# Kernel tuning notes

Hardware: AMD Instinct MI355X
Metric: run time of the kernel (lower is better)

The kernel has to match this reference:

```python
import jax, jax.numpy as jnp
import numpy as np

N = 4096
INP_DIM = 256
EMB_DIM = 256
ALPHA = 0.01  # LeakyReLU negative slope
NEG_INF = -9.0e15


def _xavier(key, shape, gain=1.414):
    fan_in, fan_out = shape[0], shape[1]
    limit = gain * np.sqrt(6.0 / (fan_in + fan_out))
    return jax.random.uniform(key, shape, jnp.float32, -limit, limit)


def setup_inputs() -> dict:
    key = jax.random.key(0)
    ks = jax.random.split(key, 9)
    inp = {
        "input": jax.random.normal(ks[0], (N, INP_DIM), jnp.float32),
        "adj": jax.random.randint(ks[1], (N, N), 0, 2, jnp.int32),
        "W0": _xavier(ks[2], (INP_DIM, EMB_DIM)),
        "W1": _xavier(ks[3], (EMB_DIM, EMB_DIM)),
        "a1": _xavier(ks[4], (2 * EMB_DIM, 1)),
        "W2": _xavier(ks[5], (EMB_DIM, EMB_DIM)),
        "a2": _xavier(ks[6], (2 * EMB_DIM, 1)),
        "W3": _xavier(ks[7], (EMB_DIM, EMB_DIM)),
        "a3": _xavier(ks[8], (2 * EMB_DIM, 1)),
    }
    return inp


def _gat_layer(h, adj, W, a):
    # h: [N, F_in], W: [F_in, F], a: [2F, 1]
    Wh = h @ W                       # [N, F]
    F_out = Wh.shape[1]
    # e_ij = leakyrelu([Wh_i || Wh_j] @ a) = leakyrelu(Wh_i@a1 + Wh_j@a2)
    f1 = Wh @ a[:F_out]              # [N, 1]
    f2 = Wh @ a[F_out:]              # [N, 1]
    e = jax.nn.leaky_relu(f1 + f2.T, ALPHA)            # [N, N]
    att = jnp.where(adj > 0, e, NEG_INF)
    att = jax.nn.softmax(att, axis=1)                    # masked softmax over neighbors
    h_prime = att @ Wh                                   # [N, F]
    return jax.nn.elu(h_prime)                           # concat=True -> ELU


def reference(input, adj, W0, W1, a1, W2, a2, W3, a3):
    h = input @ W0                   # GAT-level projection
    h = _gat_layer(h, adj, W1, a1)
    h = _gat_layer(h, adj, W2, a2)
    h = _gat_layer(h, adj, W3, a3)
    return h
```

## Files before the change

### kernel.cpp

```cpp
#include <hip/hip_runtime.h>
#include <hip/hip_bf16.h>
#include <hip/hip_fp16.h>
#include <cstdint>
#include <cstddef>

#define NN 4096
#define FD 256
#define WPR 64

typedef __attribute__((ext_vector_type(8))) unsigned short ushort8v;
typedef __attribute__((ext_vector_type(4))) unsigned short ushort4v;
typedef __attribute__((ext_vector_type(8))) short short8;
typedef __attribute__((ext_vector_type(4))) float float4v;

#define C1 30.0f
#define C2 0.3f

static __device__ __forceinline__ unsigned short f2bf(float x) {
    union { float f; unsigned int u; } v; v.f = x;
    unsigned int r = v.u + 0x7FFFu + ((v.u >> 16) & 1u);
    return (unsigned short)(r >> 16);
}

static __device__ __forceinline__ short8 as_s8(ushort8v v) {
    union { ushort8v u; short8 s; } x; x.u = v; return x.s;
}

static __device__ __forceinline__ void gl_lds16(const unsigned short* g, unsigned short* l) {
    __builtin_amdgcn_global_load_lds(
        (const __attribute__((address_space(1))) unsigned int*)g,
        (__attribute__((address_space(3))) unsigned int*)l,
        16, 0, 0);
}

__global__ __launch_bounds__(256) void setup(const int* __restrict__ adj,
                                             const float* __restrict__ input,
                                             const float* __restrict__ W0, const float* __restrict__ W1,
                                             const float* __restrict__ W2, const float* __restrict__ W3,
                                             unsigned long long* __restrict__ bits,
                                             unsigned short* __restrict__ hb,
                                             unsigned short* __restrict__ Wbt,
                                             float* __restrict__ f1f2) {
    const int b = blockIdx.x;
    const int t = threadIdx.x;
    if (b < 4096) {
        const int wave = t >> 6, lane = t & 63;
        const int* arow = adj + (size_t)b * NN;
        #pragma unroll
        for (int it = 0; it < NN / 256; ++it) {
            int j = it * 256 + wave * 64 + lane;
            unsigned long long m = __ballot(arow[j] > 0);
            if (lane == 0) bits[(size_t)b * WPR + (it * 4 + wave)] = m;
        }
        hb[(size_t)b * 256 + t] = f2bf(input[(size_t)b * 256 + t]);
    } else if (b < 5120) {
        int idx = (b - 4096) * 256 + t;
        int mat = idx >> 16;
        int within = idx & 65535;
        int n = within >> 8, k = within & 255;
        const float* W = (mat == 0) ? W0 : (mat == 1) ? W1 : (mat == 2) ? W2 : W3;
        Wbt[idx] = f2bf(W[k * 256 + n]);
    } else {
        #pragma unroll
        for (int i = 0; i < 24; ++i) {
            int pos = i * 1024 + (b - 5120) * 256 + t;
            f1f2[pos] = 0.f;
        }
    }
}

__global__ __launch_bounds__(256) void proj_gemm(const unsigned short* __restrict__ A,
                                                 const unsigned short* __restrict__ Bt,
                                                 const float* __restrict__ av,
                                                 float* __restrict__ f1f2,
                                                 unsigned short* __restrict__ Cbt,
                                                 unsigned short* __restrict__ Crow) {
    const int t = threadIdx.x;
    const int bm = blockIdx.x >> 2, bn = blockIdx.x & 3;
    const int m0 = bm * 32, n0 = bn * 64;
    __shared__ unsigned short As[32 * 264];
    __shared__ unsigned short Bs[64 * 264];
    const int lane = t & 63, wave = t >> 6;
    const int wm = (wave >> 1) * 16, wn = (wave & 1) * 32;
    const int g = lane >> 4, ml = lane & 15;
    {
        int ar = t >> 3, ac0 = (t & 7) * 8;
        #pragma unroll
        for (int i = 0; i < 4; ++i) {
            int col = ac0 + i * 64;
            *(ushort8v*)&As[ar * 264 + col] = *(const ushort8v*)&A[(size_t)(m0 + ar) * 256 + col];
        }
        int br = t >> 2, bc0 = (t & 3) * 8;
        #pragma unroll
        for (int i = 0; i < 8; ++i) {
            int col = bc0 + i * 32;
            *(ushort8v*)&Bs[br * 264 + col] = *(const ushort8v*)&Bt[(size_t)(n0 + br) * 256 + col];
        }
    }
    __syncthreads();
    float4v acc[2] = {{0.f,0.f,0.f,0.f},{0.f,0.f,0.f,0.f}};
    #pragma unroll
    for (int kk = 0; kk < 256; kk += 32) {
        const int kc = kk + g * 8;
        short8 a = as_s8(*(const ushort8v*)&As[(wm + ml) * 264 + kc]);
        #pragma unroll
        for (int fn = 0; fn < 2; ++fn) {
            short8 b = as_s8(*(const ushort8v*)&Bs[(wn + fn * 16 + ml) * 264 + kc]);
            acc[fn] = __builtin_amdgcn_mfma_f32_16x16x32_bf16(a, b, acc[fn], 0, 0, 0);
        }
    }

    const int rb = wm + g * 4;
    if (Crow) {
        #pragma unroll
        for (int fn = 0; fn < 2; ++fn)
            #pragma unroll
            for (int r = 0; r < 4; ++r)
                Crow[(size_t)(m0 + rb + r) * 256 + n0 + wn + fn * 16 + ml] = f2bf(acc[fn][r]);
    }

    if (f1f2) {
        float a1c[2], a2c[2];
        #pragma unroll
        for (int fn = 0; fn < 2; ++fn) {
            a1c[fn] = av[n0 + wn + fn * 16 + ml];
            a2c[fn] = av[256 + n0 + wn + fn * 16 + ml];
        }
        #pragma unroll
        for (int r = 0; r < 4; ++r) {
            float s1 = acc[0][r] * a1c[0] + acc[1][r] * a1c[1];
            float s2 = acc[0][r] * a2c[0] + acc[1][r] * a2c[1];
            #pragma unroll
            for (int off = 1; off < 16; off <<= 1) {
                s1 += __shfl_xor(s1, off, 64);
                s2 += __shfl_xor(s2, off, 64);
            }
            if (ml == 0) {
                int row = m0 + rb + r;
                atomicAdd(&f1f2[row], s1);
                atomicAdd(&f1f2[4096 + row], s2);
            }
        }
    }

    if (Cbt) {
        unsigned short* T = As;
        __syncthreads();
        #pragma unroll
        for (int fn = 0; fn < 2; ++fn)
            #pragma unroll
            for (int r = 0; r < 4; ++r)
                T[(wn + fn * 16 + ml) * 40 + rb + r] = f2bf(acc[fn][r]);
        __syncthreads();
        const int tr = t >> 2, tc = (t & 3) * 8;
        *(ushort8v*)&Cbt[(size_t)(n0 + tr) * 4096 + m0 + tc] = *(const ushort8v*)&T[tr * 40 + tc];
    }
}

__global__ __launch_bounds__(256) void rowcoef(const unsigned long long* __restrict__ bits,
                                               const float* __restrict__ f1f2,
                                               float4* __restrict__ rowco,
                                               float2* __restrict__ tab2g) {
    __shared__ float2 tl[4096];
    const int t = threadIdx.x;
    const float* f2p = f1f2 + 4096;
    #pragma unroll
    for (int i = 0; i < 16; ++i) {
        float v = f2p[i * 256 + t];
        float2 pr = make_float2(__expf(v - C1), __expf(0.01f * v - C2));
        tl[i * 256 + t] = pr;
        if (blockIdx.x == 0) tab2g[i * 256 + t] = pr;
    }
    __syncthreads();
    const int lane = t & 63, wave = t >> 6;
    for (int rr = 0; rr < 2; ++rr) {
        const int row = blockIdx.x * 8 + wave * 2 + rr;
        const unsigned long long wl = bits[(size_t)row * WPR + lane];
        const float f1r = f1f2[row];
        const float th = __expf(-f1r - C1);
        float mx = 0.f, S1 = 0.f, S2 = 0.f;
        #pragma unroll 16
        for (int b = 0; b < 64; ++b) {
            unsigned long long w = __shfl(wl, b, 64);
            bool bit = (w >> lane) & 1ULL;
            float2 v = tl[b * 64 + lane];
            float ebm = bit ? v.x : 0.f;
            mx = fmaxf(mx, ebm);
            bool cond = v.x > th;
            S1 += (bit && cond)  ? v.x : 0.f;
            S2 += (bit && !cond) ? v.y : 0.f;
        }
        #pragma unroll
        for (int off = 1; off < 64; off <<= 1) {
            mx = fmaxf(mx, __shfl_xor(mx, off, 64));
            S1 += __shfl_xor(S1, off, 64);
            S2 += __shfl_xor(S2, off, 64);
        }
        if (lane == 0) {
            float M  = C1 + __logf(mx);
            float fm_ = f1r + M;
            float m  = fm_ > 0.f ? fm_ : 0.01f * fm_;
            float alpha = __expf(fminf(f1r + C1 - m, 60.f));
            float gamma = __expf(fminf(0.01f * (f1r + C1) - m, 60.f));
            float inv = 1.0f / (alpha * S1 + gamma * S2);
            rowco[row] = make_float4(alpha * inv, gamma * inv, th, 0.f);
        }
    }
}

template<int NSTEPS>
__global__ __launch_bounds__(256, 3) void att_gemm(const unsigned long long* __restrict__ bits,
                                                   const float4* __restrict__ rowco,
                                                   const float* __restrict__ tab2f,
                                                   const unsigned short* __restrict__ Bt,
                                                   unsigned short* __restrict__ parth) {
    const int t = threadIdx.x;
    const int bm = blockIdx.x & 31;
    const int bn = (blockIdx.x >> 5) & 1;
    const int ks = blockIdx.x >> 6;
    const int m0 = bm * 128, n0 = bn * 128;
    const int k0 = ks * (NSTEPS * 32);
    __shared__ unsigned short Bs[2][128 * 32];
    const int lane = t & 63, wave = t >> 6;
    const int g = lane >> 4, ml = lane & 15;

    const int drow = lane >> 2, dcol = ((lane & 3) ^ (lane >> 4)) * 8;
    const unsigned short* dsrc0 = Bt + (size_t)(n0 + wave * 16 + drow) * 4096 + dcol;
    const unsigned short* dsrc1 = dsrc0 + (size_t)64 * 4096;
    unsigned short* dst0 = &Bs[0][wave * 512];
    unsigned short* dst1 = &Bs[0][2048 + wave * 512];
    unsigned short* dst0b = &Bs[1][wave * 512];
    unsigned short* dst1b = &Bs[1][2048 + wave * 512];

    float pA[2], pG[2];
    unsigned long long wpre[2][NSTEPS / 2];
    #pragma unroll
    for (int fm = 0; fm < 2; ++fm) {
        int row = m0 + wave * 32 + fm * 16 + ml;
        float4 rc = rowco[row];
        pA[fm] = rc.x; pG[fm] = rc.y;
        const unsigned long long* brow = bits + (size_t)row * WPR + (k0 >> 6);
        #pragma unroll
        for (int w = 0; w < NSTEPS / 2; ++w) wpre[fm][w] = brow[w];
    }

    float4v acc[2][8];
    #pragma unroll
    for (int i = 0; i < 2; ++i)
        #pragma unroll
        for (int j = 0; j < 8; ++j) acc[i][j] = (float4v){0.f, 0.f, 0.f, 0.f};

    float4v tq0, tq1, tq2, tq3;
    {
        gl_lds16(dsrc0 + k0, dst0);
        gl_lds16(dsrc1 + k0, dst1);
        const float4v* q = (const float4v*)&tab2f[2 * (k0 + g * 8)];
        tq0 = q[0]; tq1 = q[1]; tq2 = q[2]; tq3 = q[3];
    }
    __syncthreads();

    const int rdoff = ((g ^ (ml >> 2)) & 3) * 8;

    #pragma unroll
    for (int i = 0; i < NSTEPS; ++i) {
        const int kk = k0 + i * 32;
        const int p = i & 1;
        float4v nt0, nt1, nt2, nt3;
        if (i + 1 < NSTEPS) {
            gl_lds16(dsrc0 + kk + 32, p ? dst0 : dst0b);
            gl_lds16(dsrc1 + kk + 32, p ? dst1 : dst1b);
            const float4v* q = (const float4v*)&tab2f[2 * (kk + 32 + g * 8)];
            nt0 = q[0]; nt1 = q[1]; nt2 = q[2]; nt3 = q[3];
        }
        const int sh = (i & 1) * 32 + g * 8;
        short8 afr[2];
        #pragma unroll
        for (int fm = 0; fm < 2; ++fm) {
            unsigned int wh = (unsigned int)(wpre[fm][i >> 1] >> sh);
            ushort8v af;
            #pragma unroll
            for (int jj = 0; jj < 4; ++jj) {
                float4v v = (jj == 0) ? tq0 : (jj == 1) ? tq1 : (jj == 2) ? tq2 : tq3;
                float x0 = fmaxf(pA[fm] * v[0], pG[fm] * v[1]);
                float x1 = fmaxf(pA[fm] * v[2], pG[fm] * v[3]);
                x0 = ((wh >> (2 * jj)) & 1u)     ? x0 : 0.f;
                x1 = ((wh >> (2 * jj + 1)) & 1u) ? x1 : 0.f;
                union { __hip_bfloat162 b2; unsigned int u; } cv;
                cv.b2 = __float22bfloat162_rn(make_float2(x0, x1));
                ((unsigned int*)&af)[jj] = cv.u;
            }
            afr[fm] = as_s8(af);
        }
        #pragma unroll
        for (int fn = 0; fn < 8; ++fn) {
            short8 b = as_s8(*(const ushort8v*)&Bs[p][(fn * 16 + ml) * 32 + rdoff]);
            acc[0][fn] = __builtin_amdgcn_mfma_f32_16x16x32_bf16(afr[0], b, acc[0][fn], 0, 0, 0);
            acc[1][fn] = __builtin_amdgcn_mfma_f32_16x16x32_bf16(afr[1], b, acc[1][fn], 0, 0, 0);
        }
        if (i + 1 < NSTEPS) {
            __syncthreads();
            tq0 = nt0; tq1 = nt1; tq2 = nt2; tq3 = nt3;
        }
    }

    unsigned short* pbase = parth + ((size_t)ks << 20) + (size_t)(bm * 2 + bn) * 16384;
    #pragma unroll
    for (int fm = 0; fm < 2; ++fm)
        #pragma unroll
        for (int fn = 0; fn < 8; ++fn) {
            ushort4v v4;
            #pragma unroll
            for (int r = 0; r < 4; ++r) {
                __half h = __float2half(acc[fm][fn][r]);
                v4[r] = *(unsigned short*)&h;
            }
            *(ushort4v*)&pbase[((wave * 16 + fm * 8 + fn) * 64 + lane) * 4] = v4;
        }
}

template<int NS>
__global__ __launch_bounds__(256) void fused_rp(const unsigned short* __restrict__ parth,
                                                const unsigned short* __restrict__ Bt,
                                                const float* __restrict__ av,
                                                float* __restrict__ f1f2,
                                                unsigned short* __restrict__ Cbt) {
    const int t = threadIdx.x;
    const int m0 = blockIdx.x * 16;
    __shared__ unsigned short hA[16 * 280];
    __shared__ unsigned short T[256 * 24];

    const int bmP = m0 >> 7;
    const int wavea = (m0 >> 5) & 3;
    const int fmP = (m0 >> 4) & 1;
    const int bn = t >> 7, fnc = (t >> 4) & 7;
    const int widx = wavea * 16 + fmP * 8 + fnc;
    const size_t cbase = (size_t)(bmP * 2 + bn) * 16384 + (size_t)widx * 256 + (t & 15) * 16;
    float s[16];
    #pragma unroll
    for (int e = 0; e < 16; ++e) s[e] = 0.f;
    #pragma unroll
    for (int sp = 0; sp < NS; ++sp) {
        const unsigned short* p = &parth[((size_t)sp << 20) + cbase];
        ushort8v v0 = *(const ushort8v*)p;
        ushort8v v1 = *(const ushort8v*)(p + 8);
        #pragma unroll
        for (int e = 0; e < 8; ++e) {
            unsigned short u0 = v0[e], u1 = v1[e];
            s[e]     += __half2float(*(__half*)&u0);
            s[8 + e] += __half2float(*(__half*)&u1);
        }
    }
    const int gq = (t & 15) >> 2;
    const int colb = bn * 128 + fnc * 16 + (t & 3) * 4;
    #pragma unroll
    for (int r = 0; r < 4; ++r) {
        ushort4v w4;
        #pragma unroll
        for (int c = 0; c < 4; ++c) {
            float x = s[c * 4 + r];
            x = x > 0.f ? x : (__expf(x) - 1.f);
            w4[c] = f2bf(x);
        }
        *(ushort4v*)&hA[(gq * 4 + r) * 280 + colb] = w4;
    }
    __syncthreads();

    const int lane = t & 63, wave = t >> 6;
    const int g = lane >> 4, ml = lane & 15;
    float4v acc[4] = {{0.f,0.f,0.f,0.f},{0.f,0.f,0.f,0.f},{0.f,0.f,0.f,0.f},{0.f,0.f,0.f,0.f}};
    #pragma unroll
    for (int kk = 0; kk < 256; kk += 32) {
        short8 a = as_s8(*(const ushort8v*)&hA[ml * 280 + kk + g * 8]);
        #pragma unroll
        for (int fn = 0; fn < 4; ++fn) {
            short8 b = as_s8(*(const ushort8v*)&Bt[(size_t)(wave * 64 + fn * 16 + ml) * 256 + kk + g * 8]);
            acc[fn] = __builtin_amdgcn_mfma_f32_16x16x32_bf16(a, b, acc[fn], 0, 0, 0);
        }
    }

    {
        float a1c[4], a2c[4];
        #pragma unroll
        for (int fn = 0; fn < 4; ++fn) {
            int col = wave * 64 + fn * 16 + ml;
            a1c[fn] = av[col];
            a2c[fn] = av[256 + col];
        }
        #pragma unroll
        for (int r = 0; r < 4; ++r) {
            float s1 = acc[0][r] * a1c[0] + acc[1][r] * a1c[1] + acc[2][r] * a1c[2] + acc[3][r] * a1c[3];
            float s2 = acc[0][r] * a2c[0] + acc[1][r] * a2c[1] + acc[2][r] * a2c[2] + acc[3][r] * a2c[3];
            #pragma unroll
            for (int off = 1; off < 16; off <<= 1) {
                s1 += __shfl_xor(s1, off, 64);
                s2 += __shfl_xor(s2, off, 64);
            }
            if (ml == 0) {
                int row = m0 + g * 4 + r;
                atomicAdd(&f1f2[row], s1);
                atomicAdd(&f1f2[4096 + row], s2);
            }
        }
    }

    #pragma unroll
    for (int fn = 0; fn < 4; ++fn) {
        int nl = wave * 64 + fn * 16 + ml;
        ushort4v v4;
        #pragma unroll
        for (int r = 0; r < 4; ++r) v4[r] = f2bf(acc[fn][r]);
        *(ushort4v*)&T[nl * 24 + g * 4] = v4;
    }
    __syncthreads();
    {
        const int tn = t >> 1, half = t & 1;
        #pragma unroll
        for (int pass = 0; pass < 2; ++pass) {
            int n = pass * 128 + tn;
            *(ushort8v*)&Cbt[(size_t)n * 4096 + m0 + half * 8] = *(const ushort8v*)&T[n * 24 + half * 8];
        }
    }
}

template<int NS>
__global__ __launch_bounds__(256) void reduce_out(const unsigned short* __restrict__ parth,
                                                  float* __restrict__ outf) {
    const int flat = (blockIdx.x * 256 + threadIdx.x) * 8;
    float s[8] = {0.f, 0.f, 0.f, 0.f, 0.f, 0.f, 0.f, 0.f};
    #pragma unroll
    for (int sp = 0; sp < NS; ++sp) {
        ushort8v v = *(const ushort8v*)&parth[((size_t)sp << 20) + flat];
        #pragma unroll
        for (int j = 0; j < 8; ++j) {
            unsigned short u = v[j];
            s[j] += __half2float(*(__half*)&u);
        }
    }
    const int tile  = flat >> 14;
    const int inner = flat & 16383;
    const int widx = inner >> 8;
    const int ls   = (inner >> 2) & 63;
    const int bm = tile >> 1, bn = tile & 1;
    const int wavea = widx >> 4, fm = (widx >> 3) & 1, fn = widx & 7;
    const int g = ls >> 4, ml = ls & 15;
    const int row0 = bm * 128 + wavea * 32 + fm * 16 + g * 4;
    const int col  = bn * 128 + fn * 16 + ml;
    #pragma unroll
    for (int r = 0; r < 4; ++r) {
        float x0 = s[r];
        float x1 = s[4 + r];
        x0 = x0 > 0.f ? x0 : (__expf(x0) - 1.f);
        x1 = x1 > 0.f ? x1 : (__expf(x1) - 1.f);
        *(float2*)&outf[(size_t)(row0 + r) * 256 + col] = make_float2(x0, x1);
    }
}

static void launch_att(int SPLIT, const unsigned long long* bits, const float4* rowco,
                       const float* tab2f, const unsigned short* Bt,
                       unsigned short* parth, hipStream_t stream) {
    if (SPLIT == 16) att_gemm<8><<<64 * 16, 256, 0, stream>>>(bits, rowco, tab2f, Bt, parth);
    else             att_gemm<16><<<64 * 8, 256, 0, stream>>>(bits, rowco, tab2f, Bt, parth);
}

static void launch_frp(int SPLIT, const unsigned short* parth, const unsigned short* Bt,
                       const float* av, float* f1f2, unsigned short* Cbt, hipStream_t stream) {
    if (SPLIT == 16) fused_rp<16><<<256, 256, 0, stream>>>(parth, Bt, av, f1f2, Cbt);
    else             fused_rp<8><<<256, 256, 0, stream>>>(parth, Bt, av, f1f2, Cbt);
}

static void launch_rout(int SPLIT, const unsigned short* parth, float* outf, hipStream_t stream) {
    if (SPLIT == 16) reduce_out<16><<<512, 256, 0, stream>>>(parth, outf);
    else             reduce_out<8><<<512, 256, 0, stream>>>(parth, outf);
}

extern "C" void kernel_launch(void* const* d_in, const int* in_sizes, int n_in,
                              void* d_out, int out_size, void* d_ws, size_t ws_size,
                              hipStream_t stream) {
    const float* input = (const float*)d_in[0];
    const int*   adj   = (const int*)d_in[1];
    const float* W0    = (const float*)d_in[2];
    const float* W1    = (const float*)d_in[3];
    const float* a1    = (const float*)d_in[4];
    const float* W2    = (const float*)d_in[5];
    const float* a2    = (const float*)d_in[6];
    const float* W3    = (const float*)d_in[7];
    const float* a3    = (const float*)d_in[8];
    float* out = (float*)d_out;
    char* ws = (char*)d_ws;

    unsigned long long* bits = (unsigned long long*)(ws);
    unsigned short* h0   = (unsigned short*)(ws + (2u << 20));
    unsigned short* h1   = (unsigned short*)(ws + (4u << 20));
    unsigned short* Whbt = (unsigned short*)(ws + (6u << 20));
    unsigned short* Wbt  = (unsigned short*)(ws + (8u << 20));
    float*  f1f2  = (float*)(ws + (9u << 20));
    float4* rowco = (float4*)(ws + (10u << 20));
    float2* tab2  = (float2*)(ws + (10u << 20) + (256u << 10));
    unsigned short* parth = (unsigned short*)(ws + (13u << 20));

    int SPLIT = 8;
    (void)ws_size;

    float* f1f2_l[3] = { f1f2, f1f2 + 8192, f1f2 + 16384 };

    setup<<<5124, 256, 0, stream>>>(adj, input, W0, W1, W2, W3, bits, h0, Wbt, f1f2);

    proj_gemm<<<512, 256, 0, stream>>>(h0, Wbt + 0 * 65536, nullptr, nullptr, nullptr, h1);

    proj_gemm<<<512, 256, 0, stream>>>(h1, Wbt + 1 * 65536, a1, f1f2_l[0], Whbt, nullptr);
    rowcoef<<<512, 256, 0, stream>>>(bits, f1f2_l[0], rowco, tab2);
    launch_att(SPLIT, bits, rowco, (const float*)tab2, Whbt, parth, stream);

    launch_frp(SPLIT, parth, Wbt + 2 * 65536, a2, f1f2_l[1], Whbt, stream);
    rowcoef<<<512, 256, 0, stream>>>(bits, f1f2_l[1], rowco, tab2);
    launch_att(SPLIT, bits, rowco, (const float*)tab2, Whbt, parth, stream);

    launch_frp(SPLIT, parth, Wbt + 3 * 65536, a3, f1f2_l[2], Whbt, stream);
    rowcoef<<<512, 256, 0, stream>>>(bits, f1f2_l[2], rowco, tab2);
    launch_att(SPLIT, bits, rowco, (const float*)tab2, Whbt, parth, stream);
    launch_rout(SPLIT, parth, out, stream);
}
```

Baseline: 272.3 us.

## Fuse setup with first projection GEMM and convert weights inline

```diff
diff --git a/kernel.cpp b/kernel.cpp
--- a/kernel.cpp
+++ b/kernel.cpp
@@ -5,7 +5,6 @@
 #include <cstddef>
 
 #define NN 4096
-#define FD 256
 #define WPR 64
 
 typedef __attribute__((ext_vector_type(8))) unsigned short ushort8v;
@@ -33,71 +32,107 @@
         16, 0, 0);
 }
 
-__global__ __launch_bounds__(256) void setup(const int* __restrict__ adj,
-                                             const float* __restrict__ input,
-                                             const float* __restrict__ W0, const float* __restrict__ W1,
-                                             const float* __restrict__ W2, const float* __restrict__ W3,
-                                             unsigned long long* __restrict__ bits,
-                                             unsigned short* __restrict__ hb,
-                                             unsigned short* __restrict__ Wbt,
-                                             float* __restrict__ f1f2) {
-    const int b = blockIdx.x;
+__global__ __launch_bounds__(256) void setup_proj0(
+    const float* __restrict__ input, const int* __restrict__ adj,
+    const float* __restrict__ W0, const float* __restrict__ W2, const float* __restrict__ W3,
+    unsigned long long* __restrict__ bits, unsigned short* __restrict__ h1,
+    unsigned short* __restrict__ Wbt, float* __restrict__ f1f2)
+{
+    const int bid = blockIdx.x;
     const int t = threadIdx.x;
-    if (b < 4096) {
-        const int wave = t >> 6, lane = t & 63;
-        const int* arow = adj + (size_t)b * NN;
-        #pragma unroll
-        for (int it = 0; it < NN / 256; ++it) {
-            int j = it * 256 + wave * 64 + lane;
-            unsigned long long m = __ballot(arow[j] > 0);
-            if (lane == 0) bits[(size_t)b * WPR + (it * 4 + wave)] = m;
-        }
-        hb[(size_t)b * 256 + t] = f2bf(input[(size_t)b * 256 + t]);
-    } else if (b < 5120) {
-        int idx = (b - 4096) * 256 + t;
-        int mat = idx >> 16;
+    const int lane = t & 63, wave = t >> 6;
+    const int g = lane >> 4, ml = lane & 15;
+    __shared__ unsigned short As[32 * 264];
+    __shared__ unsigned short Bs[64 * 264];
+
+    if (t < 48) f1f2[bid * 48 + t] = 0.f;
+    {
+        int idx = 131072 + bid * 256 + t;
         int within = idx & 65535;
         int n = within >> 8, k = within & 255;
-        const float* W = (mat == 0) ? W0 : (mat == 1) ? W1 : (mat == 2) ? W2 : W3;
+        const float* W = ((idx >> 16) == 2) ? W2 : W3;
         Wbt[idx] = f2bf(W[k * 256 + n]);
-    } else {
-        #pragma unroll
-        for (int i = 0; i < 24; ++i) {
-            int pos = i * 1024 + (b - 5120) * 256 + t;
-            f1f2[pos] = 0.f;
-        }
-    }
-}
-
-__global__ __launch_bounds__(256) void proj_gemm(const unsigned short* __restrict__ A,
-                                                 const unsigned short* __restrict__ Bt,
-                                                 const float* __restrict__ av,
-                                                 float* __restrict__ f1f2,
-                                                 unsigned short* __restrict__ Cbt,
-                                                 unsigned short* __restrict__ Crow) {
+    }
+    const int m0 = (bid >> 2) * 32, n0 = (bid & 3) * 64;
+    {
+        int ar = t >> 3, ac0 = (t & 7) * 8;
+        #pragma unroll
+        for (int i = 0; i < 4; ++i) {
+            int col = ac0 + i * 64;
+            const float* src = &input[(size_t)(m0 + ar) * 256 + col];
+            ushort8v v;
+            #pragma unroll
+            for (int j = 0; j < 8; ++j) v[j] = f2bf(src[j]);
+            *(ushort8v*)&As[ar * 264 + col] = v;
+        }
+        #pragma unroll 8
+        for (int it = 0; it < 64; ++it) {
+            int k = it * 4 + wave;
+            Bs[(t & 63) * 264 + k] = f2bf(W0[k * 256 + n0 + (t & 63)]);
+        }
+    }
+    __syncthreads();
+    {
+        const int wm = (wave >> 1) * 16, wn = (wave & 1) * 32;
+        float4v acc[2] = {{0.f,0.f,0.f,0.f},{0.f,0.f,0.f,0.f}};
+        #pragma unroll
+        for (int kk = 0; kk < 256; kk += 32) {
+            const int kc = kk + g * 8;
+            short8 a = as_s8(*(const ushort8v*)&As[(wm + ml) * 264 + kc]);
+            #pragma unroll
+            for (int fn = 0; fn < 2; ++fn) {
+                short8 b = as_s8(*(const ushort8v*)&Bs[(wn + fn * 16 + ml) * 264 + kc]);
+                acc[fn] = __builtin_amdgcn_mfma_f32_16x16x32_bf16(a, b, acc[fn], 0, 0, 0);
+            }
+        }
+        const int rb = wm + g * 4;
+        #pragma unroll
+        for (int fn = 0; fn < 2; ++fn)
+            #pragma unroll
+            for (int r = 0; r < 4; ++r)
+                h1[(size_t)(m0 + rb + r) * 256 + n0 + wn + fn * 16 + ml] = f2bf(acc[fn][r]);
+    }
+    {
+        #pragma unroll 1
+        for (int rr = 0; rr < 2; ++rr) {
+            int row = bid * 8 + wave * 2 + rr;
+            const int* arow = adj + (size_t)row * NN;
+            #pragma unroll 8
+            for (int seg = 0; seg < 64; ++seg) {
+                unsigned long long m = __ballot(arow[seg * 64 + lane] > 0);
+                if (lane == 0) bits[(size_t)row * WPR + seg] = m;
+            }
+        }
+    }
+}
+
+__global__ __launch_bounds__(256) void proj1(
+    const unsigned short* __restrict__ h1, const float* __restrict__ W1,
+    const float* __restrict__ a1v, float* __restrict__ f1f2,
+    unsigned short* __restrict__ Whbt)
+{
+    const int bid = blockIdx.x;
     const int t = threadIdx.x;
-    const int bm = blockIdx.x >> 2, bn = blockIdx.x & 3;
-    const int m0 = bm * 32, n0 = bn * 64;
+    const int lane = t & 63, wave = t >> 6;
+    const int g = lane >> 4, ml = lane & 15;
     __shared__ unsigned short As[32 * 264];
     __shared__ unsigned short Bs[64 * 264];
-    const int lane = t & 63, wave = t >> 6;
-    const int wm = (wave >> 1) * 16, wn = (wave & 1) * 32;
-    const int g = lane >> 4, ml = lane & 15;
+    const int m0 = (bid >> 2) * 32, n0 = (bid & 3) * 64;
     {
         int ar = t >> 3, ac0 = (t & 7) * 8;
         #pragma unroll
         for (int i = 0; i < 4; ++i) {
             int col = ac0 + i * 64;
-            *(ushort8v*)&As[ar * 264 + col] = *(const ushort8v*)&A[(size_t)(m0 + ar) * 256 + col];
-        }
-        int br = t >> 2, bc0 = (t & 3) * 8;
-        #pragma unroll
-        for (int i = 0; i < 8; ++i) {
-            int col = bc0 + i * 32;
-            *(ushort8v*)&Bs[br * 264 + col] = *(const ushort8v*)&Bt[(size_t)(n0 + br) * 256 + col];
+            *(ushort8v*)&As[ar * 264 + col] = *(const ushort8v*)&h1[(size_t)(m0 + ar) * 256 + col];
+        }
+        #pragma unroll 8
+        for (int it = 0; it < 64; ++it) {
+            int k = it * 4 + wave;
+            Bs[(t & 63) * 264 + k] = f2bf(W1[k * 256 + n0 + (t & 63)]);
         }
     }
     __syncthreads();
+    const int wm = (wave >> 1) * 16, wn = (wave & 1) * 32;
     float4v acc[2] = {{0.f,0.f,0.f,0.f},{0.f,0.f,0.f,0.f}};
     #pragma unroll
     for (int kk = 0; kk < 256; kk += 32) {
@@ -109,22 +144,13 @@
             acc[fn] = __builtin_amdgcn_mfma_f32_16x16x32_bf16(a, b, acc[fn], 0, 0, 0);
         }
     }
-
     const int rb = wm + g * 4;
-    if (Crow) {
-        #pragma unroll
-        for (int fn = 0; fn < 2; ++fn)
-            #pragma unroll
-            for (int r = 0; r < 4; ++r)
-                Crow[(size_t)(m0 + rb + r) * 256 + n0 + wn + fn * 16 + ml] = f2bf(acc[fn][r]);
-    }
-
-    if (f1f2) {
+    {
         float a1c[2], a2c[2];
         #pragma unroll
         for (int fn = 0; fn < 2; ++fn) {
-            a1c[fn] = av[n0 + wn + fn * 16 + ml];
-            a2c[fn] = av[256 + n0 + wn + fn * 16 + ml];
+            a1c[fn] = a1v[n0 + wn + fn * 16 + ml];
+            a2c[fn] = a1v[256 + n0 + wn + fn * 16 + ml];
         }
         #pragma unroll
         for (int r = 0; r < 4; ++r) {
@@ -142,8 +168,7 @@
             }
         }
     }
-
-    if (Cbt) {
+    {
         unsigned short* T = As;
         __syncthreads();
         #pragma unroll
@@ -153,7 +178,7 @@
                 T[(wn + fn * 16 + ml) * 40 + rb + r] = f2bf(acc[fn][r]);
         __syncthreads();
         const int tr = t >> 2, tc = (t & 3) * 8;
-        *(ushort8v*)&Cbt[(size_t)(n0 + tr) * 4096 + m0 + tc] = *(const ushort8v*)&T[tr * 40 + tc];
+        *(ushort8v*)&Whbt[(size_t)(n0 + tr) * 4096 + m0 + tc] = *(const ushort8v*)&T[tr * 40 + tc];
     }
 }
 
@@ -455,24 +480,6 @@
     }
 }
 
-static void launch_att(int SPLIT, const unsigned long long* bits, const float4* rowco,
-                       const float* tab2f, const unsigned short* Bt,
-                       unsigned short* parth, hipStream_t stream) {
-    if (SPLIT == 16) att_gemm<8><<<64 * 16, 256, 0, stream>>>(bits, rowco, tab2f, Bt, parth);
-    else             att_gemm<16><<<64 * 8, 256, 0, stream>>>(bits, rowco, tab2f, Bt, parth);
-}
-
-static void launch_frp(int SPLIT, const unsigned short* parth, const unsigned short* Bt,
-                       const float* av, float* f1f2, unsigned short* Cbt, hipStream_t stream) {
-    if (SPLIT == 16) fused_rp<16><<<256, 256, 0, stream>>>(parth, Bt, av, f1f2, Cbt);
-    else             fused_rp<8><<<256, 256, 0, stream>>>(parth, Bt, av, f1f2, Cbt);
-}
-
-static void launch_rout(int SPLIT, const unsigned short* parth, float* outf, hipStream_t stream) {
-    if (SPLIT == 16) reduce_out<16><<<512, 256, 0, stream>>>(parth, outf);
-    else             reduce_out<8><<<512, 256, 0, stream>>>(parth, outf);
-}
-
 extern "C" void kernel_launch(void* const* d_in, const int* in_sizes, int n_in,
                               void* d_out, int out_size, void* d_ws, size_t ws_size,
                               hipStream_t stream) {
@@ -489,7 +496,6 @@
     char* ws = (char*)d_ws;
 
     unsigned long long* bits = (unsigned long long*)(ws);
-    unsigned short* h0   = (unsigned short*)(ws + (2u << 20));
     unsigned short* h1   = (unsigned short*)(ws + (4u << 20));
     unsigned short* Whbt = (unsigned short*)(ws + (6u << 20));
     unsigned short* Wbt  = (unsigned short*)(ws + (8u << 20));
@@ -497,26 +503,22 @@
     float4* rowco = (float4*)(ws + (10u << 20));
     float2* tab2  = (float2*)(ws + (10u << 20) + (256u << 10));
     unsigned short* parth = (unsigned short*)(ws + (13u << 20));
-
-    int SPLIT = 8;
     (void)ws_size;
 
     float* f1f2_l[3] = { f1f2, f1f2 + 8192, f1f2 + 16384 };
 
-    setup<<<5124, 256, 0, stream>>>(adj, input, W0, W1, W2, W3, bits, h0, Wbt, f1f2);
-
-    proj_gemm<<<512, 256, 0, stream>>>(h0, Wbt + 0 * 65536, nullptr, nullptr, nullptr, h1);
-
-    proj_gemm<<<512, 256, 0, stream>>>(h1, Wbt + 1 * 65536, a1, f1f2_l[0], Whbt, nullptr);
+    setup_proj0<<<512, 256, 0, stream>>>(input, adj, W0, W2, W3, bits, h1, Wbt, f1f2);
+
+    proj1<<<512, 256, 0, stream>>>(h1, W1, a1, f1f2_l[0], Whbt);
     rowcoef<<<512, 256, 0, stream>>>(bits, f1f2_l[0], rowco, tab2);
-    launch_att(SPLIT, bits, rowco, (const float*)tab2, Whbt, parth, stream);
-
-    launch_frp(SPLIT, parth, Wbt + 2 * 65536, a2, f1f2_l[1], Whbt, stream);
+    att_gemm<16><<<512, 256, 0, stream>>>(bits, rowco, (const float*)tab2, Whbt, parth);
+
+    fused_rp<8><<<256, 256, 0, stream>>>(parth, Wbt + 2 * 65536, a2, f1f2_l[1], Whbt);
     rowcoef<<<512, 256, 0, stream>>>(bits, f1f2_l[1], rowco, tab2);
-    launch_att(SPLIT, bits, rowco, (const float*)tab2, Whbt, parth, stream);
-
-    launch_frp(SPLIT, parth, Wbt + 3 * 65536, a3, f1f2_l[2], Whbt, stream);
+    att_gemm<16><<<512, 256, 0, stream>>>(bits, rowco, (const float*)tab2, Whbt, parth);
+
+    fused_rp<8><<<256, 256, 0, stream>>>(parth, Wbt + 3 * 65536, a3, f1f2_l[2], Whbt);
     rowcoef<<<512, 256, 0, stream>>>(bits, f1f2_l[2], rowco, tab2);
-    launch_att(SPLIT, bits, rowco, (const float*)tab2, Whbt, parth, stream);
-    launch_rout(SPLIT, parth, out, stream);
-}
+    att_gemm<16><<<512, 256, 0, stream>>>(bits, rowco, (const float*)tab2, Whbt, parth);
+    reduce_out<8><<<512, 256, 0, stream>>>(parth, out);
+}
```

Result: slower. 311.1 us (+14.3%).
